# Performance work log

Measured on AMD Instinct MI355X. Metric: run time of the kernel, lower is better.

## Reference

```python
import jax, jax.numpy as jnp
import numpy as np

IMG = 224
PATCH = 16
CH = 3
D_DIM = 768
ROW = IMG // PATCH            # 14
N_PATCHES = ROW * ROW         # 196
PATCH_DIM = PATCH * PATCH * CH  # 768


def setup_inputs() -> dict:
    key = jax.random.key(0)
    k1, k2, k3 = jax.random.split(key, 3)
    x = jax.random.normal(k1, (32, CH, IMG, IMG), dtype=jnp.float32)
    # stacked per-patch Linear weights: torch nn.Linear(in=PATCH_DIM, out=D_DIM)
    # weight shape [out, in]; we store [n_patches, in, out] for batched einsum
    bound = 1.0 / np.sqrt(PATCH_DIM)
    W = jax.random.uniform(k2, (N_PATCHES, PATCH_DIM, D_DIM), dtype=jnp.float32,
                           minval=-bound, maxval=bound)
    b = jax.random.uniform(k3, (N_PATCHES, D_DIM), dtype=jnp.float32,
                           minval=-bound, maxval=bound)
    return {"x": x, "W": W, "b": b}


def _extract_patches(x):
    # x: [B, C, H, W] -> [B, n_patches, C*p*p] matching torch crop+Flatten order
    B = x.shape[0]
    x = x.reshape(B, CH, ROW, PATCH, ROW, PATCH)          # [B,C,r,p,c,p]
    x = x.transpose(0, 2, 4, 1, 3, 5)                     # [B,r,c,C,p,p]
    return x.reshape(B, N_PATCHES, PATCH_DIM)


def reference(x, W, b):
    patches = _extract_patches(x)                         # [B, N, P]
    # per-patch independent linear: one batched GEMM over the patch axis
    out = jnp.einsum('bnp,npd->bnd', patches, W) + b      # [B, N, D]
    return out
```

## Files before the change

kernel.cpp:

```cpp
#include <hip/hip_runtime.h>

#define IMG 224
#define PATCHSZ 16
#define CHN 3
#define DDIM 768
#define ROWN 14
#define NPATCH 196
#define PDIM 768
#define BATCH 32

#define DTILE 256
#define NDBLK (DDIM / DTILE)
#define KCHUNK 64
#define NCHUNK (PDIM / KCHUNK)
#define KSUB 16
#define NSUB (PDIM / KSUB)

__global__ void extract_patches_kernel(const float* __restrict__ x,
                                       float* __restrict__ P) {
    int i = blockIdx.x * blockDim.x + threadIdx.x;
    if (i >= NPATCH * BATCH * PDIM) return;
    int k  = i % PDIM;
    int nb = i / PDIM;
    int b  = nb % BATCH;
    int n  = nb / BATCH;
    int ch = k >> 8;
    int py = (k >> 4) & 15;
    int px = k & 15;
    int r = n / ROWN, c = n % ROWN;
    P[i] = x[(((size_t)b * CHN + ch) * IMG + r * PATCHSZ + py) * IMG
             + c * PATCHSZ + px];
}

#define PK_FMA_LO(a2, w2, p2)                                                \
    asm("v_pk_fma_f32 %0, %1, %2, %0 op_sel:[0,0,0] op_sel_hi:[1,0,1]"       \
        : "+v"(a2) : "v"(w2), "v"(p2))
#define PK_FMA_HI(a2, w2, p2)                                                \
    asm("v_pk_fma_f32 %0, %1, %2, %0 op_sel:[0,1,0] op_sel_hi:[1,1,1]"       \
        : "+v"(a2) : "v"(w2), "v"(p2))

__global__ __launch_bounds__(256, 2) void patch_gemm_kernel(
    const float* __restrict__ P,
    const float* __restrict__ W,
    const float* __restrict__ bias,
    float* __restrict__ out)
{
    __shared__ __align__(16) float wt[2][KSUB][DTILE];
    __shared__ __align__(16) float ap[2][KCHUNK][BATCH];

    const int blk  = blockIdx.x;
    const int n    = blk / NDBLK;
    const int dblk = blk % NDBLK;
    const int tid  = threadIdx.x;
    const int ln   = tid & 63;
    const int wv   = tid >> 6;
    const int b0   = wv * 8;
    const int d    = dblk * DTILE + ln * 4;

    const float* Wn0 = W + (size_t)n * PDIM * DDIM + dblk * DTILE;
    const float* Pn  = P + (size_t)n * BATCH * PDIM;

    const int sb = tid >> 3;
    const int sk = (tid & 7) * 8;

    float2 acc[8][2];
#pragma unroll
    for (int i = 0; i < 8; ++i) {
        acc[i][0] = make_float2(0.f, 0.f);
        acc[i][1] = make_float2(0.f, 0.f);
    }

    auto issueW = [&](int u) {
        const float* src = Wn0 + (size_t)u * KSUB * DDIM;
        float* dst = &wt[u & 1][0][0];
#pragma unroll
        for (int j = 0; j < 4; ++j) {
            const int row = wv * 4 + j;
            __builtin_amdgcn_global_load_lds(
                (const __attribute__((address_space(1))) unsigned int*)
                    (src + (size_t)row * DDIM + ln * 4),
                (__attribute__((address_space(3))) unsigned int*)
                    (dst + row * DTILE + ln * 4),
                16, 0, 0);
        }
    };

    {
        const float* s = Pn + (size_t)sb * PDIM + sk;
        float4 v0 = *reinterpret_cast<const float4*>(s);
        float4 v1 = *reinterpret_cast<const float4*>(s + 4);
        float (*apb)[BATCH] = ap[0];
        apb[sk + 0][sb] = v0.x; apb[sk + 1][sb] = v0.y;
        apb[sk + 2][sb] = v0.z; apb[sk + 3][sb] = v0.w;
        apb[sk + 4][sb] = v1.x; apb[sk + 5][sb] = v1.y;
        apb[sk + 6][sb] = v1.z; apb[sk + 7][sb] = v1.w;
    }
    float4 pn0, pn1;
    {
        const float* s = Pn + (size_t)sb * PDIM + KCHUNK + sk;
        pn0 = *reinterpret_cast<const float4*>(s);
        pn1 = *reinterpret_cast<const float4*>(s + 4);
    }
    issueW(0);

#pragma unroll 1
    for (int u = 0; u < NSUB; ++u) {
        __syncthreads();
        if (u + 1 < NSUB) issueW(u + 1);

        const int c  = u >> 2;
        const int kb = (u & 3) * KSUB;
        const float* wbuf = &wt[u & 1][0][0] + ln * 4;
        const float* pbuf = &ap[c & 1][0][0] + b0;

#pragma unroll 4
        for (int kk = 0; kk < KSUB; ++kk) {
            const float* wp = wbuf + kk * DTILE;
            float2 wlo = *reinterpret_cast<const float2*>(wp);
            float2 whi = *reinterpret_cast<const float2*>(wp + 2);
            const float* pp = pbuf + (size_t)(kb + kk) * BATCH;
            float2 p01 = *reinterpret_cast<const float2*>(pp);
            float2 p23 = *reinterpret_cast<const float2*>(pp + 2);
            float2 p45 = *reinterpret_cast<const float2*>(pp + 4);
            float2 p67 = *reinterpret_cast<const float2*>(pp + 6);

            PK_FMA_LO(acc[0][0], wlo, p01); PK_FMA_LO(acc[0][1], whi, p01);
            PK_FMA_HI(acc[1][0], wlo, p01); PK_FMA_HI(acc[1][1], whi, p01);
            PK_FMA_LO(acc[2][0], wlo, p23); PK_FMA_LO(acc[2][1], whi, p23);
            PK_FMA_HI(acc[3][0], wlo, p23); PK_FMA_HI(acc[3][1], whi, p23);
            PK_FMA_LO(acc[4][0], wlo, p45); PK_FMA_LO(acc[4][1], whi, p45);
            PK_FMA_HI(acc[5][0], wlo, p45); PK_FMA_HI(acc[5][1], whi, p45);
            PK_FMA_LO(acc[6][0], wlo, p67); PK_FMA_LO(acc[6][1], whi, p67);
            PK_FMA_HI(acc[7][0], wlo, p67); PK_FMA_HI(acc[7][1], whi, p67);
        }

        if ((u & 3) == 3 && c + 1 < NCHUNK) {
            float (*apb)[BATCH] = ap[(c + 1) & 1];
            apb[sk + 0][sb] = pn0.x; apb[sk + 1][sb] = pn0.y;
            apb[sk + 2][sb] = pn0.z; apb[sk + 3][sb] = pn0.w;
            apb[sk + 4][sb] = pn1.x; apb[sk + 5][sb] = pn1.y;
            apb[sk + 6][sb] = pn1.z; apb[sk + 7][sb] = pn1.w;
            if (c + 2 < NCHUNK) {
                const float* s = Pn + (size_t)sb * PDIM + (c + 2) * KCHUNK + sk;
                pn0 = *reinterpret_cast<const float4*>(s);
                pn1 = *reinterpret_cast<const float4*>(s + 4);
            }
        }
    }

    float4 bv = *reinterpret_cast<const float4*>(bias + (size_t)n * DDIM + d);
#pragma unroll
    for (int i = 0; i < 8; ++i) {
        const int b = b0 + i;
        float4 o;
        o.x = acc[i][0].x + bv.x;
        o.y = acc[i][0].y + bv.y;
        o.z = acc[i][1].x + bv.z;
        o.w = acc[i][1].y + bv.w;
        *reinterpret_cast<float4*>(out + ((size_t)b * NPATCH + n) * DDIM + d) = o;
    }
}

extern "C" void kernel_launch(void* const* d_in, const int* in_sizes, int n_in,
                              void* d_out, int out_size, void* d_ws, size_t ws_size,
                              hipStream_t stream) {
    const float* x    = (const float*)d_in[0];
    const float* W    = (const float*)d_in[1];
    const float* bias = (const float*)d_in[2];
    float* out = (float*)d_out;
    float* P   = (float*)d_ws;

    int total = NPATCH * BATCH * PDIM;
    extract_patches_kernel<<<(total + 255) / 256, 256, 0, stream>>>(x, P);
    patch_gemm_kernel<<<NPATCH * NDBLK, 256, 0, stream>>>(P, W, bias, out);
}
```

Baseline: 165.7 us.

## Halve GEMM D-tile to 128 with 128-thread blocks and XCD-aware block remap

The D tile shrinks from 256 to 128 columns and each block now has 2 waves of 128 threads instead of 4, so the grid doubles to 1176 blocks and fills the CUs better. Thread-to-data mappings for the W LDS loads, the P staging and the compute lanes are rewritten to match. Block IDs are also remapped so that consecutive workgroups on the same XCD handle neighbouring patches, which should improve L2 locality. In exchange, each block re-reads the P patch tile twice as often per output and carries less latency hiding per CU.

```diff
diff --git a/kernel.cpp b/kernel.cpp
--- a/kernel.cpp
+++ b/kernel.cpp
@@ -9,12 +9,13 @@
 #define PDIM 768
 #define BATCH 32
 
-#define DTILE 256
+#define DTILE 128
 #define NDBLK (DDIM / DTILE)
 #define KCHUNK 64
 #define NCHUNK (PDIM / KCHUNK)
 #define KSUB 16
 #define NSUB (PDIM / KSUB)
+#define NWG (NPATCH * NDBLK)
 
 __global__ void extract_patches_kernel(const float* __restrict__ x,
                                        float* __restrict__ P) {
@@ -39,7 +40,7 @@
     asm("v_pk_fma_f32 %0, %1, %2, %0 op_sel:[0,1,0] op_sel_hi:[1,1,1]"       \
         : "+v"(a2) : "v"(w2), "v"(p2))
 
-__global__ __launch_bounds__(256, 2) void patch_gemm_kernel(
+__global__ __launch_bounds__(128, 2) void patch_gemm_kernel(
     const float* __restrict__ P,
     const float* __restrict__ W,
     const float* __restrict__ bias,
@@ -48,20 +49,21 @@
     __shared__ __align__(16) float wt[2][KSUB][DTILE];
     __shared__ __align__(16) float ap[2][KCHUNK][BATCH];
 
-    const int blk  = blockIdx.x;
-    const int n    = blk / NDBLK;
-    const int dblk = blk % NDBLK;
-    const int tid  = threadIdx.x;
-    const int ln   = tid & 63;
-    const int wv   = tid >> 6;
-    const int b0   = wv * 8;
-    const int d    = dblk * DTILE + ln * 4;
+    const int wid  = (blockIdx.x & 7) * (NWG / 8) + (blockIdx.x >> 3);
+    const int n    = wid / NDBLK;
+    const int dblk = wid % NDBLK;
+    const int t    = threadIdx.x;
+    const int l    = t & 63;
+    const int wv   = t >> 6;
+    const int dq   = t & 31;
+    const int b0   = (t >> 5) * 8;
+    const int d    = dblk * DTILE + dq * 4;
 
     const float* Wn0 = W + (size_t)n * PDIM * DDIM + dblk * DTILE;
     const float* Pn  = P + (size_t)n * BATCH * PDIM;
 
-    const int sb = tid >> 3;
-    const int sk = (tid & 7) * 8;
+    const int sb = t >> 2;
+    const int sk = (t & 3) * 16;
 
     float2 acc[8][2];
 #pragma unroll
@@ -75,31 +77,35 @@
         float* dst = &wt[u & 1][0][0];
 #pragma unroll
         for (int j = 0; j < 4; ++j) {
-            const int row = wv * 4 + j;
+            const int row = j * 4 + wv * 2 + (l >> 5);
+            const int col = (l & 31) * 4;
             __builtin_amdgcn_global_load_lds(
                 (const __attribute__((address_space(1))) unsigned int*)
-                    (src + (size_t)row * DDIM + ln * 4),
+                    (src + (size_t)row * DDIM + col),
                 (__attribute__((address_space(3))) unsigned int*)
-                    (dst + row * DTILE + ln * 4),
+                    (dst + row * DTILE + col),
                 16, 0, 0);
         }
     };
 
     {
         const float* s = Pn + (size_t)sb * PDIM + sk;
-        float4 v0 = *reinterpret_cast<const float4*>(s);
-        float4 v1 = *reinterpret_cast<const float4*>(s + 4);
         float (*apb)[BATCH] = ap[0];
-        apb[sk + 0][sb] = v0.x; apb[sk + 1][sb] = v0.y;
-        apb[sk + 2][sb] = v0.z; apb[sk + 3][sb] = v0.w;
-        apb[sk + 4][sb] = v1.x; apb[sk + 5][sb] = v1.y;
-        apb[sk + 6][sb] = v1.z; apb[sk + 7][sb] = v1.w;
+#pragma unroll
+        for (int j = 0; j < 4; ++j) {
+            float4 v = *reinterpret_cast<const float4*>(s + j * 4);
+            apb[sk + j * 4 + 0][sb] = v.x;
+            apb[sk + j * 4 + 1][sb] = v.y;
+            apb[sk + j * 4 + 2][sb] = v.z;
+            apb[sk + j * 4 + 3][sb] = v.w;
+        }
     }
-    float4 pn0, pn1;
+    float4 pn[4];
     {
         const float* s = Pn + (size_t)sb * PDIM + KCHUNK + sk;
-        pn0 = *reinterpret_cast<const float4*>(s);
-        pn1 = *reinterpret_cast<const float4*>(s + 4);
+#pragma unroll
+        for (int j = 0; j < 4; ++j)
+            pn[j] = *reinterpret_cast<const float4*>(s + j * 4);
     }
     issueW(0);
 
@@ -110,7 +116,7 @@
 
         const int c  = u >> 2;
         const int kb = (u & 3) * KSUB;
-        const float* wbuf = &wt[u & 1][0][0] + ln * 4;
+        const float* wbuf = &wt[u & 1][0][0] + dq * 4;
         const float* pbuf = &ap[c & 1][0][0] + b0;
 
 #pragma unroll 4
@@ -136,14 +142,18 @@
 
         if ((u & 3) == 3 && c + 1 < NCHUNK) {
             float (*apb)[BATCH] = ap[(c + 1) & 1];
-            apb[sk + 0][sb] = pn0.x; apb[sk + 1][sb] = pn0.y;
-            apb[sk + 2][sb] = pn0.z; apb[sk + 3][sb] = pn0.w;
-            apb[sk + 4][sb] = pn1.x; apb[sk + 5][sb] = pn1.y;
-            apb[sk + 6][sb] = pn1.z; apb[sk + 7][sb] = pn1.w;
+#pragma unroll
+            for (int j = 0; j < 4; ++j) {
+                apb[sk + j * 4 + 0][sb] = pn[j].x;
+                apb[sk + j * 4 + 1][sb] = pn[j].y;
+                apb[sk + j * 4 + 2][sb] = pn[j].z;
+                apb[sk + j * 4 + 3][sb] = pn[j].w;
+            }
             if (c + 2 < NCHUNK) {
                 const float* s = Pn + (size_t)sb * PDIM + (c + 2) * KCHUNK + sk;
-                pn0 = *reinterpret_cast<const float4*>(s);
-                pn1 = *reinterpret_cast<const float4*>(s + 4);
+#pragma unroll
+                for (int j = 0; j < 4; ++j)
+                    pn[j] = *reinterpret_cast<const float4*>(s + j * 4);
             }
         }
     }
@@ -172,5 +182,5 @@
 
     int total = NPATCH * BATCH * PDIM;
     extract_patches_kernel<<<(total + 255) / 256, 256, 0, stream>>>(x, P);
-    patch_gemm_kernel<<<NPATCH * NDBLK, 256, 0, stream>>>(P, W, bias, out);
+    patch_gemm_kernel<<<NWG, 128, 0, stream>>>(P, W, bias, out);
 }
```

Measured after the change: 208.5 us (median of 2 runs). 25.8% more time.
